# Kernel tuning notes

Hardware: AMD Instinct MI355X
Metric: run time of the kernel (lower is better)

## Reference

```python
import jax, jax.numpy as jnp
import numpy as np

B, S, D, H = 2, 2048, 1024, 16
HD = D // H  # head_dim = 64
THETA = 10000.0


def setup_inputs() -> dict:
    key = jax.random.key(0)
    ks = jax.random.split(key, 7)
    sd = 1.0 / np.sqrt(D)
    return {
        "hidden_states": jax.random.normal(ks[0], (B, S, D), jnp.float32),
        "attention_mask": jnp.ones((B, S), jnp.int32),
        "Wq": jax.random.normal(ks[1], (D, D), jnp.float32) * sd,
        "Wk": jax.random.normal(ks[2], (D, D), jnp.float32) * sd,
        "Wv": jax.random.normal(ks[3], (D, D), jnp.float32) * sd,
        "Wo": jax.random.normal(ks[4], (D, D), jnp.float32) * sd,
        "bo": jnp.zeros((D,), jnp.float32),
        "rel_bias": jax.random.normal(ks[5], (H, S, S), jnp.float32) * 0.02,
    }


def _rope_tables(seq_len):
    inv_freq = 1.0 / (THETA ** (jnp.arange(0, HD, 2, dtype=jnp.float32) / HD))  # [HD/2]
    freqs = jnp.arange(seq_len, dtype=jnp.float32)[:, None] * inv_freq[None, :]  # [S, HD/2]
    # add a heads axis for broadcasting against [B, S, H, HD/2]
    return jnp.cos(freqs)[:, None, :], jnp.sin(freqs)[:, None, :]


def _apply_rope(x, cos, sin):
    # x: [B, S, H, HD]; interleaved even/odd rotation
    x1, x2 = x[..., 0::2], x[..., 1::2]
    r1 = x1 * cos - x2 * sin
    r2 = x1 * sin + x2 * cos
    return jnp.stack([r1, r2], axis=-1).reshape(x.shape)


def reference(hidden_states, attention_mask, Wq, Wk, Wv, Wo, bo, rel_bias):
    b, s, d = hidden_states.shape
    q = (hidden_states @ Wq.T).reshape(b, s, H, HD)
    k = (hidden_states @ Wk.T).reshape(b, s, H, HD)
    v = (hidden_states @ Wv.T).reshape(b, s, H, HD)

    cos, sin = _rope_tables(s)
    q = _apply_rope(q, cos, sin)
    k = _apply_rope(k, cos, sin)

    scale = HD ** -0.5
    scores = jnp.einsum('bqhd,bkhd->bhqk', q, k) * scale + rel_bias[None]
    scores = jnp.where(attention_mask[:, None, None, :] == 0, -jnp.inf, scores)
    attn = jax.nn.softmax(scores, axis=-1)  # dropout is identity in eval
    out = jnp.einsum('bhqk,bkhd->bqhd', attn, v).reshape(b, s, d)
    return out @ Wo.T + bo
```

## Files before the change

kernel.cpp:

```cpp
#include <hip/hip_runtime.h>

typedef unsigned short u16;
typedef short bf16x8 __attribute__((ext_vector_type(8)));
typedef float f32x4 __attribute__((ext_vector_type(4)));
typedef unsigned short u16x4 __attribute__((ext_vector_type(4)));

typedef const __attribute__((address_space(1))) unsigned int* gas_ptr;
typedef __attribute__((address_space(3))) unsigned int* las_ptr;

__device__ __forceinline__ void gl_lds16(const void* g, void* l) {
  __builtin_amdgcn_global_load_lds((gas_ptr)g, (las_ptr)l, 16, 0, 0);
}

__device__ __forceinline__ u16 f2bf(float f) {
  union { float f; unsigned u; } v; v.f = f;
  unsigned r = v.u + 0x7FFFu + ((v.u >> 16) & 1u);
  return (u16)(r >> 16);
}

__global__ void k_rope_tables(float* __restrict__ ctab, float* __restrict__ stab) {
  int t = blockIdx.x * 256 + threadIdx.x;
  int s = t >> 5, tt = t & 31;
  double f = exp(-((double)(2 * tt) / 64.0) * log(10000.0));
  double a = (double)s * f;
  ctab[t] = (float)cos(a);
  stab[t] = (float)sin(a);
}

__device__ __forceinline__ void store_bf4(u16* p, float4 v) {
  u16x4 o; o[0] = f2bf(v.x); o[1] = f2bf(v.y); o[2] = f2bf(v.z); o[3] = f2bf(v.w);
  *(u16x4*)p = o;
}

__global__ void k_convert(const float* __restrict__ hs, const float* __restrict__ Wq,
                          const float* __restrict__ Wk, const float* __restrict__ Wv,
                          const float* __restrict__ Wo,
                          u16* __restrict__ Xb, u16* __restrict__ Wqkv, u16* __restrict__ Wob) {
  int e = (blockIdx.x * 256 + threadIdx.x) * 4;
  const int R1 = 4096 * 1024, R2 = R1 + 3072 * 1024;
  if (e < R1) {
    store_bf4(Xb + e, *(const float4*)&hs[e]);
  } else if (e < R2) {
    int w = e - R1; int row = w >> 10, col = w & 1023;
    const float* src = row < 1024 ? &Wq[(size_t)row * 1024]
                     : (row < 2048 ? &Wk[(size_t)(row - 1024) * 1024]
                                   : &Wv[(size_t)(row - 2048) * 1024]);
    store_bf4(Wqkv + w, *(const float4*)&src[col]);
  } else {
    int w = e - R2;
    store_bf4(Wob + w, *(const float4*)&Wo[w]);
  }
}

__global__ __launch_bounds__(256, 2)
void k_gemm_bt(const u16* __restrict__ A, const u16* __restrict__ B,
               const float* __restrict__ bias, float* __restrict__ C,
               int K, int ldc) {
  __shared__ u16 ldsA[128 * 64];
  __shared__ u16 ldsB[128 * 64];
  const int tid = threadIdx.x;
  const int bn = blockIdx.x, bm = blockIdx.y;
  const int lane = tid & 63, wave = tid >> 6;
  const int wm = wave >> 1, wn = wave & 1;
  const int l16 = lane & 15, quad = lane >> 4;

  const int srow = lane >> 3, scol = (lane & 7) * 8;
  const u16* agb = A + (size_t)(bm * 128 + wave * 8 + srow) * K + scol;
  const u16* bgb = B + (size_t)(bn * 128 + wave * 8 + srow) * K + scol;

  const f32x4 vzero = {0.f, 0.f, 0.f, 0.f};
  f32x4 acc[4][4];
#pragma unroll
  for (int i = 0; i < 4; ++i)
#pragma unroll
    for (int j = 0; j < 4; ++j) acc[i][j] = vzero;

  const int NKT = K >> 6;
  for (int kt = 0; kt < NKT; ++kt) {
    __syncthreads();
#pragma unroll
    for (int p = 0; p < 4; ++p) {
      gl_lds16(agb + (size_t)p * 32 * K + kt * 64, &ldsA[(p * 4 + wave) * 512]);
      gl_lds16(bgb + (size_t)p * 32 * K + kt * 64, &ldsB[(p * 4 + wave) * 512]);
    }
    __syncthreads();
#pragma unroll
    for (int ks = 0; ks < 2; ++ks) {
      bf16x8 af[4], bfr[4];
#pragma unroll
      for (int mi = 0; mi < 4; ++mi)
        af[mi] = *(const bf16x8*)&ldsA[(wm * 64 + mi * 16 + l16) * 64 + ks * 32 + quad * 8];
#pragma unroll
      for (int ni = 0; ni < 4; ++ni)
        bfr[ni] = *(const bf16x8*)&ldsB[(wn * 64 + ni * 16 + l16) * 64 + ks * 32 + quad * 8];
#pragma unroll
      for (int mi = 0; mi < 4; ++mi)
#pragma unroll
        for (int ni = 0; ni < 4; ++ni)
          acc[mi][ni] = __builtin_amdgcn_mfma_f32_16x16x32_bf16(af[mi], bfr[ni], acc[mi][ni], 0, 0, 0);
    }
  }

  const int row0 = bm * 128 + wm * 64, col0 = bn * 128 + wn * 64;
#pragma unroll
  for (int mi = 0; mi < 4; ++mi)
#pragma unroll
    for (int ni = 0; ni < 4; ++ni) {
      int col = col0 + ni * 16 + l16;
      float badd = bias ? bias[col] : 0.f;
#pragma unroll
      for (int rr = 0; rr < 4; ++rr) {
        int row = row0 + mi * 16 + quad * 4 + rr;
        C[(size_t)row * ldc + col] = acc[mi][ni][rr] + badd;
      }
    }
}

__global__ void k_rope_apply(const float* __restrict__ QKV, const float* __restrict__ ctab,
                             const float* __restrict__ stab,
                             u16* __restrict__ Qb, u16* __restrict__ Kb) {
  int t = blockIdx.x * 256 + threadIdx.x;
  int i = t >> 9;
  int c = t & 511; int h = c >> 5, tt = c & 31;
  int s = i & 2047, b = i >> 11;
  const float* base = QKV + (size_t)i * 3072;
  float cs = ctab[s * 32 + tt], sn = stab[s * 32 + tt];
  float q0 = base[h * 64 + 2 * tt], q1 = base[h * 64 + 2 * tt + 1];
  float k0 = base[1024 + h * 64 + 2 * tt], k1 = base[1024 + h * 64 + 2 * tt + 1];
  size_t ob = ((size_t)(b * 16 + h) * 2048 + s) * 64 + 2 * tt;
  Qb[ob]     = f2bf((q0 * cs - q1 * sn) * 0.125f);
  Qb[ob + 1] = f2bf((q0 * sn + q1 * cs) * 0.125f);
  Kb[ob]     = f2bf(k0 * cs - k1 * sn);
  Kb[ob + 1] = f2bf(k0 * sn + k1 * cs);
}

__global__ void k_vtrans(const float* __restrict__ QKV, u16* __restrict__ Vtb) {
  __shared__ u16 T[64 * 72];
  int st = blockIdx.x & 31, bh = blockIdx.x >> 5;
  int tid = threadIdx.x;
  int b = bh >> 4, h = bh & 15;
  {
    int rr = tid >> 2;
    int dg = (tid & 3) * 16;
    const float* src = QKV + (size_t)(b * 2048 + st * 64 + rr) * 3072 + 2048 + h * 64 + dg;
#pragma unroll
    for (int j = 0; j < 4; ++j) {
      float4 v = *(const float4*)&src[j * 4];
      T[(dg + j * 4 + 0) * 72 + rr] = f2bf(v.x);
      T[(dg + j * 4 + 1) * 72 + rr] = f2bf(v.y);
      T[(dg + j * 4 + 2) * 72 + rr] = f2bf(v.z);
      T[(dg + j * 4 + 3) * 72 + rr] = f2bf(v.w);
    }
  }
  __syncthreads();
  int d = tid >> 2, cg = (tid & 3) * 2;
  u16* vo = Vtb + ((size_t)bh * 64 + d) * 2048 + st * 64;
  *(float4*)&vo[cg * 8]       = *(const float4*)&T[d * 72 + cg * 8];
  *(float4*)&vo[(cg + 1) * 8] = *(const float4*)&T[d * 72 + (cg + 1) * 8];
}

#define PSTR 68
__global__ __launch_bounds__(256, 4)
void k_attn(const u16* __restrict__ Qb, const u16* __restrict__ Kb, const u16* __restrict__ Vtb,
            const float* __restrict__ rel_bias, const int* __restrict__ mask,
            u16* __restrict__ Ob) {
  __shared__ u16 Ks[64 * 64];
  __shared__ u16 Vs[64 * 64];
  __shared__ u16 Ps[64 * PSTR];

  const int tid = threadIdx.x;
  const int gid = blockIdx.x;
  const int b = gid & 1, h = (gid >> 1) & 15, qt = gid >> 5;
  const int bh = b * 16 + h;
  const int lane = tid & 63, w = tid >> 6;
  const int l16 = lane & 15, quad = lane >> 4;

  bf16x8 qreg[2];
  {
    const u16* qg = Qb + ((size_t)bh * 2048 + qt * 64 + w * 16 + l16) * 64 + quad * 8;
    qreg[0] = *(const bf16x8*)&qg[0];
    qreg[1] = *(const bf16x8*)&qg[32];
  }

  const int srow = lane >> 3, scol = (lane & 7) * 8;
  const u16* kgb = Kb + ((size_t)bh * 2048 + w * 8 + srow) * 64 + scol;
  const u16* vgb = Vtb + ((size_t)bh * 64 + w * 8 + srow) * 2048 + scol;

  const float* bp[4];
#pragma unroll
  for (int rr = 0; rr < 4; ++rr)
    bp[rr] = rel_bias + ((size_t)h * 2048 + qt * 64 + w * 16 + quad * 4 + rr) * 2048 + l16;
  const int* mbase = mask + b * 2048 + l16;

  const f32x4 vzero = {0.f, 0.f, 0.f, 0.f};
  f32x4 accO[4];
  float ls[4] = {0.f, 0.f, 0.f, 0.f};
#pragma unroll
  for (int ni = 0; ni < 4; ++ni) accO[ni] = vzero;

  for (int kt0 = 0; kt0 < 2048; kt0 += 64) {
    __syncthreads();
    gl_lds16(kgb + kt0 * 64,        &Ks[(0 * 4 + w) * 512]);
    gl_lds16(kgb + kt0 * 64 + 2048, &Ks[(1 * 4 + w) * 512]);
    gl_lds16(vgb + kt0,             &Vs[(0 * 4 + w) * 512]);
    gl_lds16(vgb + kt0 + 32 * 2048, &Vs[(1 * 4 + w) * 512]);
    float breg[4][4];
    int mk[4];
#pragma unroll
    for (int ni = 0; ni < 4; ++ni) {
      mk[ni] = mbase[kt0 + ni * 16];
#pragma unroll
      for (int rr = 0; rr < 4; ++rr) breg[ni][rr] = bp[rr][kt0 + ni * 16];
    }
    __syncthreads();

    f32x4 sa[4];
#pragma unroll
    for (int ni = 0; ni < 4; ++ni) sa[ni] = vzero;
#pragma unroll
    for (int ks = 0; ks < 2; ++ks) {
#pragma unroll
      for (int ni = 0; ni < 4; ++ni) {
        bf16x8 kf = *(const bf16x8*)&Ks[(ni * 16 + l16) * 64 + ks * 32 + quad * 8];
        sa[ni] = __builtin_amdgcn_mfma_f32_16x16x32_bf16(qreg[ks], kf, sa[ni], 0, 0, 0);
      }
    }

#pragma unroll
    for (int ni = 0; ni < 4; ++ni) {
#pragma unroll
      for (int rr = 0; rr < 4; ++rr) {
        float p = mk[ni] ? __expf(sa[ni][rr] + breg[ni][rr] - 24.f) : 0.f;
        Ps[(w * 16 + quad * 4 + rr) * PSTR + ni * 16 + l16] = f2bf(p);
        ls[rr] += p;
      }
    }
    __syncthreads();

#pragma unroll
    for (int ks = 0; ks < 2; ++ks) {
      bf16x8 pf = *(const bf16x8*)&Ps[(w * 16 + l16) * PSTR + ks * 32 + quad * 8];
#pragma unroll
      for (int ni = 0; ni < 4; ++ni) {
        bf16x8 vf = *(const bf16x8*)&Vs[(ni * 16 + l16) * 64 + ks * 32 + quad * 8];
        accO[ni] = __builtin_amdgcn_mfma_f32_16x16x32_bf16(pf, vf, accO[ni], 0, 0, 0);
      }
    }
  }

#pragma unroll
  for (int rr = 0; rr < 4; ++rr) {
#pragma unroll
    for (int d = 1; d < 16; d <<= 1) ls[rr] += __shfl_xor(ls[rr], d, 16);
  }
#pragma unroll
  for (int rr = 0; rr < 4; ++rr) {
    float inv = 1.f / ls[rr];
    int row = qt * 64 + w * 16 + quad * 4 + rr;
#pragma unroll
    for (int ni = 0; ni < 4; ++ni)
      Ob[(((size_t)b * 2048 + row) * 16 + h) * 64 + ni * 16 + l16] = f2bf(accO[ni][rr] * inv);
  }
}

extern "C" void kernel_launch(void* const* d_in, const int* in_sizes, int n_in,
                              void* d_out, int out_size, void* d_ws, size_t ws_size,
                              hipStream_t stream) {
  (void)in_sizes; (void)n_in; (void)out_size; (void)ws_size;
  const float* hs  = (const float*)d_in[0];
  const int*   msk = (const int*)d_in[1];
  const float* Wq  = (const float*)d_in[2];
  const float* Wk  = (const float*)d_in[3];
  const float* Wv  = (const float*)d_in[4];
  const float* Wo  = (const float*)d_in[5];
  const float* bo  = (const float*)d_in[6];
  const float* rb  = (const float*)d_in[7];
  float* out = (float*)d_out;

  char* ws = (char*)d_ws;
  size_t off = 0;
  auto alloc = [&](size_t n) { char* p = ws + off; off += (n + 255) & ~(size_t)255; return p; };
  float* QKV  = (float*)alloc(4096UL * 3072 * 4);
  u16*   Xb   = (u16*)  alloc(4096UL * 1024 * 2);
  u16*   Wqkv = (u16*)  alloc(3072UL * 1024 * 2);
  u16*   Wob  = (u16*)  alloc(1024UL * 1024 * 2);
  u16*   Qb   = (u16*)  alloc(4096UL * 1024 * 2);
  u16*   Kb   = (u16*)  alloc(4096UL * 1024 * 2);
  u16*   Vtb  = (u16*)  alloc(4096UL * 1024 * 2);
  float* ctab = (float*)alloc(2048UL * 32 * 4);
  float* stab = (float*)alloc(2048UL * 32 * 4);
  u16*   Ob   = Xb;

  k_rope_tables<<<256, 256, 0, stream>>>(ctab, stab);
  k_convert<<<8192, 256, 0, stream>>>(hs, Wq, Wk, Wv, Wo, Xb, Wqkv, Wob);
  k_gemm_bt<<<dim3(24, 32), 256, 0, stream>>>(Xb, Wqkv, nullptr, QKV, 1024, 3072);
  k_rope_apply<<<8192, 256, 0, stream>>>(QKV, ctab, stab, Qb, Kb);
  k_vtrans<<<1024, 256, 0, stream>>>(QKV, Vtb);
  k_attn<<<1024, 256, 0, stream>>>(Qb, Kb, Vtb, rb, msk, Ob);
  k_gemm_bt<<<dim3(8, 32), 256, 0, stream>>>(Ob, Wob, bo, out, 1024, 1024);
}
```

Measured before the change: 543.1 us.

## Double-buffer attention K/V tiles, XOR-swizzle LDS layouts, vectorize RoPE stores

The attention kernel now keeps two LDS buffers for K and V. Each iteration prefetches the next tile's K/V along with its bias and mask values while it computes on the current tile, which removes one barrier per iteration and hides global load latency. Both the GEMM and the attention kernels use an XOR swizzle on the 16-byte column chunks in LDS to cut bank conflicts on the MFMA fragment reads. The RoPE kernel switches to float2 loads and packed 32-bit bf16 stores. The cost is twice the K/V LDS footprint and more registers for the prefetched bias, and the attention launch bound drops from 4 to 3 blocks per CU, which may lower occupancy.

```diff
diff --git a/kernel.cpp b/kernel.cpp
--- a/kernel.cpp
+++ b/kernel.cpp
@@ -64,7 +64,8 @@
   const int wm = wave >> 1, wn = wave & 1;
   const int l16 = lane & 15, quad = lane >> 4;
 
-  const int srow = lane >> 3, scol = (lane & 7) * 8;
+  const int srow = lane >> 3;
+  const int scol = ((lane & 7) ^ srow) * 8;
   const u16* agb = A + (size_t)(bm * 128 + wave * 8 + srow) * K + scol;
   const u16* bgb = B + (size_t)(bn * 128 + wave * 8 + srow) * K + scol;
 
@@ -75,6 +76,7 @@
 #pragma unroll
     for (int j = 0; j < 4; ++j) acc[i][j] = vzero;
 
+  const int xq = l16 & 7;
   const int NKT = K >> 6;
   for (int kt = 0; kt < NKT; ++kt) {
     __syncthreads();
@@ -89,10 +91,10 @@
       bf16x8 af[4], bfr[4];
 #pragma unroll
       for (int mi = 0; mi < 4; ++mi)
-        af[mi] = *(const bf16x8*)&ldsA[(wm * 64 + mi * 16 + l16) * 64 + ks * 32 + quad * 8];
+        af[mi] = *(const bf16x8*)&ldsA[(wm * 64 + mi * 16 + l16) * 64 + ((ks * 4 + quad) ^ xq) * 8];
 #pragma unroll
       for (int ni = 0; ni < 4; ++ni)
-        bfr[ni] = *(const bf16x8*)&ldsB[(wn * 64 + ni * 16 + l16) * 64 + ks * 32 + quad * 8];
+        bfr[ni] = *(const bf16x8*)&ldsB[(wn * 64 + ni * 16 + l16) * 64 + ((ks * 4 + quad) ^ xq) * 8];
 #pragma unroll
       for (int mi = 0; mi < 4; ++mi)
 #pragma unroll
@@ -125,13 +127,16 @@
   int s = i & 2047, b = i >> 11;
   const float* base = QKV + (size_t)i * 3072;
   float cs = ctab[s * 32 + tt], sn = stab[s * 32 + tt];
-  float q0 = base[h * 64 + 2 * tt], q1 = base[h * 64 + 2 * tt + 1];
-  float k0 = base[1024 + h * 64 + 2 * tt], k1 = base[1024 + h * 64 + 2 * tt + 1];
+  float2 q = *(const float2*)&base[h * 64 + 2 * tt];
+  float2 k = *(const float2*)&base[1024 + h * 64 + 2 * tt];
   size_t ob = ((size_t)(b * 16 + h) * 2048 + s) * 64 + 2 * tt;
-  Qb[ob]     = f2bf((q0 * cs - q1 * sn) * 0.125f);
-  Qb[ob + 1] = f2bf((q0 * sn + q1 * cs) * 0.125f);
-  Kb[ob]     = f2bf(k0 * cs - k1 * sn);
-  Kb[ob + 1] = f2bf(k0 * sn + k1 * cs);
+  union { u16 h2[2]; unsigned u; } oq, ok;
+  oq.h2[0] = f2bf((q.x * cs - q.y * sn) * 0.125f);
+  oq.h2[1] = f2bf((q.x * sn + q.y * cs) * 0.125f);
+  ok.h2[0] = f2bf(k.x * cs - k.y * sn);
+  ok.h2[1] = f2bf(k.x * sn + k.y * cs);
+  *(unsigned*)&Qb[ob] = oq.u;
+  *(unsigned*)&Kb[ob] = ok.u;
 }
 
 __global__ void k_vtrans(const float* __restrict__ QKV, u16* __restrict__ Vtb) {
@@ -160,12 +165,12 @@
 }
 
 #define PSTR 68
-__global__ __launch_bounds__(256, 4)
+__global__ __launch_bounds__(256, 3)
 void k_attn(const u16* __restrict__ Qb, const u16* __restrict__ Kb, const u16* __restrict__ Vtb,
             const float* __restrict__ rel_bias, const int* __restrict__ mask,
             u16* __restrict__ Ob) {
-  __shared__ u16 Ks[64 * 64];
-  __shared__ u16 Vs[64 * 64];
+  __shared__ u16 Ks[2][64 * 64];
+  __shared__ u16 Vs[2][64 * 64];
   __shared__ u16 Ps[64 * PSTR];
 
   const int tid = threadIdx.x;
@@ -174,6 +179,7 @@
   const int bh = b * 16 + h;
   const int lane = tid & 63, w = tid >> 6;
   const int l16 = lane & 15, quad = lane >> 4;
+  const int xq = l16 & 7;
 
   bf16x8 qreg[2];
   {
@@ -182,7 +188,8 @@
     qreg[1] = *(const bf16x8*)&qg[32];
   }
 
-  const int srow = lane >> 3, scol = (lane & 7) * 8;
+  const int srow = lane >> 3;
+  const int scol = ((lane & 7) ^ srow) * 8;
   const u16* kgb = Kb + ((size_t)bh * 2048 + w * 8 + srow) * 64 + scol;
   const u16* vgb = Vtb + ((size_t)bh * 64 + w * 8 + srow) * 2048 + scol;
 
@@ -198,39 +205,54 @@
 #pragma unroll
   for (int ni = 0; ni < 4; ++ni) accO[ni] = vzero;
 
-  for (int kt0 = 0; kt0 < 2048; kt0 += 64) {
+  float brc[4][4], brn[4][4];
+  int mkc[4], mkn[4];
+#pragma unroll
+  for (int ni = 0; ni < 4; ++ni) {
+    mkc[ni] = mbase[ni * 16];
+#pragma unroll
+    for (int rr = 0; rr < 4; ++rr) brc[ni][rr] = bp[rr][ni * 16];
+  }
+  gl_lds16(kgb,               &Ks[0][(0 * 4 + w) * 512]);
+  gl_lds16(kgb + 2048,        &Ks[0][(1 * 4 + w) * 512]);
+  gl_lds16(vgb,               &Vs[0][(0 * 4 + w) * 512]);
+  gl_lds16(vgb + 32 * 2048,   &Vs[0][(1 * 4 + w) * 512]);
+
+  for (int t = 0; t < 32; ++t) {
+    const int cur = t & 1, nxt = cur ^ 1;
+    const int kt0 = t * 64;
     __syncthreads();
-    gl_lds16(kgb + kt0 * 64,        &Ks[(0 * 4 + w) * 512]);
-    gl_lds16(kgb + kt0 * 64 + 2048, &Ks[(1 * 4 + w) * 512]);
-    gl_lds16(vgb + kt0,             &Vs[(0 * 4 + w) * 512]);
-    gl_lds16(vgb + kt0 + 32 * 2048, &Vs[(1 * 4 + w) * 512]);
-    float breg[4][4];
-    int mk[4];
+
+    if (t + 1 < 32) {
+      gl_lds16(kgb + (kt0 + 64) * 64,        &Ks[nxt][(0 * 4 + w) * 512]);
+      gl_lds16(kgb + (kt0 + 64) * 64 + 2048, &Ks[nxt][(1 * 4 + w) * 512]);
+      gl_lds16(vgb + kt0 + 64,               &Vs[nxt][(0 * 4 + w) * 512]);
+      gl_lds16(vgb + kt0 + 64 + 32 * 2048,   &Vs[nxt][(1 * 4 + w) * 512]);
+#pragma unroll
+      for (int ni = 0; ni < 4; ++ni) {
+        mkn[ni] = mbase[kt0 + 64 + ni * 16];
+#pragma unroll
+        for (int rr = 0; rr < 4; ++rr) brn[ni][rr] = bp[rr][kt0 + 64 + ni * 16];
+      }
+    }
+
+    f32x4 sa[4];
+#pragma unroll
+    for (int ni = 0; ni < 4; ++ni) sa[ni] = vzero;
+#pragma unroll
+    for (int ks = 0; ks < 2; ++ks) {
+#pragma unroll
+      for (int ni = 0; ni < 4; ++ni) {
+        bf16x8 kf = *(const bf16x8*)&Ks[cur][(ni * 16 + l16) * 64 + ((ks * 4 + quad) ^ xq) * 8];
+        sa[ni] = __builtin_amdgcn_mfma_f32_16x16x32_bf16(qreg[ks], kf, sa[ni], 0, 0, 0);
+      }
+    }
+
 #pragma unroll
     for (int ni = 0; ni < 4; ++ni) {
-      mk[ni] = mbase[kt0 + ni * 16];
-#pragma unroll
-      for (int rr = 0; rr < 4; ++rr) breg[ni][rr] = bp[rr][kt0 + ni * 16];
-    }
-    __syncthreads();
-
-    f32x4 sa[4];
-#pragma unroll
-    for (int ni = 0; ni < 4; ++ni) sa[ni] = vzero;
-#pragma unroll
-    for (int ks = 0; ks < 2; ++ks) {
-#pragma unroll
-      for (int ni = 0; ni < 4; ++ni) {
-        bf16x8 kf = *(const bf16x8*)&Ks[(ni * 16 + l16) * 64 + ks * 32 + quad * 8];
-        sa[ni] = __builtin_amdgcn_mfma_f32_16x16x32_bf16(qreg[ks], kf, sa[ni], 0, 0, 0);
-      }
-    }
-
-#pragma unroll
-    for (int ni = 0; ni < 4; ++ni) {
 #pragma unroll
       for (int rr = 0; rr < 4; ++rr) {
-        float p = mk[ni] ? __expf(sa[ni][rr] + breg[ni][rr] - 24.f) : 0.f;
+        float p = mkc[ni] ? __expf(sa[ni][rr] + brc[ni][rr] - 24.f) : 0.f;
         Ps[(w * 16 + quad * 4 + rr) * PSTR + ni * 16 + l16] = f2bf(p);
         ls[rr] += p;
       }
@@ -242,9 +264,16 @@
       bf16x8 pf = *(const bf16x8*)&Ps[(w * 16 + l16) * PSTR + ks * 32 + quad * 8];
 #pragma unroll
       for (int ni = 0; ni < 4; ++ni) {
-        bf16x8 vf = *(const bf16x8*)&Vs[(ni * 16 + l16) * 64 + ks * 32 + quad * 8];
+        bf16x8 vf = *(const bf16x8*)&Vs[cur][(ni * 16 + l16) * 64 + ((ks * 4 + quad) ^ xq) * 8];
         accO[ni] = __builtin_amdgcn_mfma_f32_16x16x32_bf16(pf, vf, accO[ni], 0, 0, 0);
       }
+    }
+
+#pragma unroll
+    for (int ni = 0; ni < 4; ++ni) {
+      mkc[ni] = mkn[ni];
+#pragma unroll
+      for (int rr = 0; rr < 4; ++rr) brc[ni][rr] = brn[ni][rr];
     }
   }
 
```

Result: no change. 553.3 us (+1.9%).
